# Kernel tuning notes

Hardware: AMD Instinct MI355X
Metric: run time of the kernel (lower is better)

Reference implementation:

```python
import jax, jax.numpy as jnp
import numpy as np

B, N, D = 4, 4096, 256

def setup_inputs() -> dict:
    key = jax.random.key(0)
    ks = jax.random.split(key, 7)
    def xavier(k, shape):
        fan_in, fan_out = shape[1], shape[0]
        a = jnp.sqrt(6.0 / (fan_in + fan_out))
        return jax.random.uniform(k, shape, jnp.float32, -a, a)
    return {
        "x": jax.random.normal(ks[0], (B, N, D), jnp.float32),
        "Wq": xavier(ks[1], (D, D)),
        "bq": jnp.zeros((D,), jnp.float32),
        "Wk": xavier(ks[2], (D, D)),
        "bk": jnp.zeros((D,), jnp.float32),
        "Wv": xavier(ks[3], (D, D)),
        "bv": jnp.zeros((D,), jnp.float32),
        "scale": jnp.asarray([jnp.sqrt(jnp.float32(D))]),
    }

def reference(x, Wq, bq, Wk, bk, Wv, bv, scale):
    # nn.Linear: y = x @ W.T + b
    q = jnp.einsum('bnd,ed->bne', x, Wq) + bq
    k = jnp.einsum('bnd,ed->bne', x, Wk) + bk
    v = jnp.einsum('bnd,ed->bne', x, Wv) + bv
    scores = jnp.einsum('bqd,bkd->bqk', q, k) / scale[0]  # [B,N,N]
    attn = jax.nn.softmax(scores, axis=-1)
    out = jnp.einsum('bqk,bkd->bqd', attn, v)
    return out
```

## Files before the change

### kernel.cpp

```cpp
#include <hip/hip_runtime.h>
#include <hip/hip_bf16.h>

typedef unsigned int u32;
typedef unsigned short u16;
typedef __attribute__((ext_vector_type(8))) __bf16 bf8v;
typedef __attribute__((ext_vector_type(16))) float f32x16;
typedef __attribute__((ext_vector_type(8))) u16 u16x8;

__device__ inline u16 f2bf(float f) {
    u32 u = __float_as_uint(f);
    u = (u + 0x7FFF + ((u >> 16) & 1)) >> 16;
    return (u16)u;
}
__device__ inline u32 pk2(float a, float b) {
    return (u32)f2bf(a) | ((u32)f2bf(b) << 16);
}
__device__ inline float bf2f(u16 h) { return __uint_as_float(((u32)h) << 16); }

__device__ inline u32 cvtpk(float a, float b) {
    u32 r;
    asm("v_cvt_pk_bf16_f32 %0, %1, %2" : "=v"(r) : "v"(a), "v"(b));
    return r;
}
__device__ inline void plswap(u32& a, u32& b) {
    asm("v_permlane32_swap_b32 %0, %1" : "+v"(a), "+v"(b));
}

__device__ inline void dma16(const u16* g, u16* l) {
    __builtin_amdgcn_global_load_lds(
        (const __attribute__((address_space(1))) void*)g,
        (__attribute__((address_space(3))) void*)l, 16, 0, 0);
}

__global__ void cvt_all(const float* __restrict__ x,
                        const float* __restrict__ wq, const float* __restrict__ wk,
                        const float* __restrict__ wv,
                        u16* __restrict__ xp, u16* __restrict__ wall) {
    const int blk = blockIdx.x;
    if (blk < 2048) {
        int g = blk * 256 + threadIdx.x;
        int row = g >> 5, cp = g & 31;
        const float* s = x + row * 256 + cp * 8;
        float4 a = *(const float4*)s;
        float4 b = *(const float4*)(s + 4);
        uint4 o;
        o.x = pk2(a.x, a.y); o.y = pk2(a.z, a.w);
        o.z = pk2(b.x, b.y); o.w = pk2(b.z, b.w);
        *(uint4*)(xp + (row >> 5) * 8192 + cp * 256 + (row & 31) * 8) = o;
    } else {
        const int bb = blk - 2048;
        const int m = bb >> 5;
        const float* src = m == 0 ? wq : m == 1 ? wk : wv;
        int g = (bb & 31) * 256 + threadIdx.x;
        int row = g >> 5, c = g & 31;
        const float* s = src + row * 256 + c * 8;
        float4 a = *(const float4*)s;
        float4 b = *(const float4*)(s + 4);
        uint4 o;
        o.x = pk2(a.x, a.y); o.y = pk2(a.z, a.w);
        o.z = pk2(b.x, b.y); o.w = pk2(b.z, b.w);
        *(uint4*)(wall + m * 65536 + row * 256 + ((c ^ (row & 7)) * 8)) = o;
    }
}

__global__ __launch_bounds__(256) void qkv_proj(
    const u16* __restrict__ xp, const u16* __restrict__ wall,
    const float* __restrict__ bq, const float* __restrict__ bk, const float* __restrict__ bv,
    const float* __restrict__ scale,
    u16* __restrict__ qp, u16* __restrict__ kp, u16* __restrict__ vp)
{
    __shared__ u16 Ws[128 * 256];

    const int blk = blockIdx.x;
    const int xcd = blk & 7;
    const int r2 = blk >> 3;
    const int rt = r2 / 6;
    const int cz = r2 % 6;
    const int sel = cz >> 1;
    const int colbase = (cz & 1) * 128;
    const int rowbase0 = (xcd * 16 + rt) * 128;

    const float* bias = sel == 0 ? bq : sel == 1 ? bk : bv;
    const float qs = sel == 0 ? 1.44269504088896f / scale[0] : 1.0f;
    const int tid = threadIdx.x;
    const int wave = tid >> 6, lane = tid & 63;
    const int l31 = lane & 31, l5 = lane >> 5;
    const int tg = (rowbase0 >> 5) + wave;

    {
        const u16* wsrc = wall + sel * 65536 + colbase * 256;
#pragma unroll
        for (int j = 0; j < 16; j++) {
            const int i = wave * 16 + j;
            dma16(wsrc + i * 512 + lane * 8, Ws + i * 512);
        }
    }
    asm volatile("s_waitcnt vmcnt(0)" ::: "memory");
    __syncthreads();

    f32x16 acc[4];
#pragma unroll
    for (int cb = 0; cb < 4; cb++)
#pragma unroll
        for (int j = 0; j < 16; j++) acc[cb][j] = 0.f;

    const u16* ap = xp + tg * 8192 + l5 * 256 + l31 * 8;
    const int sw = l31 & 7;
#pragma unroll
    for (int kk = 0; kk < 16; kk++) {
        bf8v af = *(const bf8v*)(ap + kk * 512);
        const int co = ((kk * 2 + l5) ^ sw) * 8;
#pragma unroll
        for (int cb = 0; cb < 4; cb++) {
            bf8v bfr = *(const bf8v*)(Ws + (cb * 32 + l31) * 256 + co);
            acc[cb] = __builtin_amdgcn_mfma_f32_32x32x16_bf16(af, bfr, acc[cb], 0, 0, 0);
        }
    }

    if (sel < 2) {
        u16* base = (sel == 0 ? qp : kp) + tg * 8192;
#pragma unroll
        for (int cb = 0; cb < 4; cb++) {
            const int colb = colbase + cb * 32;
            const float bc = bias[colb + l31];
            const int c0 = (colb >> 3) + (l31 >> 3), j0 = l31 & 7;
#pragma unroll
            for (int r = 0; r < 16; r++) {
                const int R = (r & 3) + 8 * (r >> 2) + 4 * l5;
                base[c0 * 256 + R * 8 + j0] = f2bf((acc[cb][r] + bc) * qs);
            }
        }
    } else {
        u16* base = vp + tg * 8192;
#pragma unroll
        for (int cb = 0; cb < 4; cb++) {
            const int colb = colbase + cb * 32;
            const float bc = bias[colb + l31];
            const int d0 = colb + l31;
#pragma unroll
            for (int r = 0; r < 16; r++) {
                const int R = (r & 3) + 8 * (r >> 2) + 4 * l5;
                base[(R >> 3) * 2048 + d0 * 8 + (R & 7)] = f2bf(acc[cb][r] + bc);
            }
        }
    }
}

__global__ __launch_bounds__(256, 2) void flash_attn(
    const u16* __restrict__ qp_, const u16* __restrict__ kp_, const u16* __restrict__ vp_,
    u16* __restrict__ Opb, float* __restrict__ ml)
{
    __shared__ u16 Ks[2 * 8192];
    __shared__ u16 Vs[2 * 8192];

    const int tid = threadIdx.x;
    const int wave = tid >> 6, lane = tid & 63;
    const int l31 = lane & 31, l5 = lane >> 5;

    const int blk = blockIdx.x;
    const int slot = blk >> 3;
    const int g = (blk & 7) * 2 + (slot >> 5);
    const int qtile = slot & 31;
    const int b = g >> 2, s = g & 3;
    const int qbase = qtile * 128 + wave * 32;

    union { u16x8 u; bf8v v; } oneu;
#pragma unroll
    for (int j = 0; j < 8; j++) oneu.u[j] = 0x3F80;
    const bf8v ones = oneu.v;

    bf8v qf[16];
    {
        const u16* qp = qp_ + (b * 128 + qtile * 4 + wave) * 8192 + l31 * 8;
#pragma unroll
        for (int kk = 0; kk < 16; kk++)
            qf[kk] = *(const bf8v*)(qp + (kk * 2 + l5) * 256);
    }

    f32x16 o[8];
#pragma unroll
    for (int i = 0; i < 8; i++)
#pragma unroll
        for (int j = 0; j < 16; j++) o[i][j] = 0.f;
    f32x16 ls;
#pragma unroll
    for (int j = 0; j < 16; j++) ls[j] = 0.f;

    const u16* kbase = kp_ + (b * 128 + s * 32) * 8192;
    const u16* vbase = vp_ + (b * 128 + s * 32) * 8192;

#pragma unroll
    for (int j = 0; j < 4; j++) {
        const int i = wave * 4 + j;
        dma16(kbase + i * 512 + lane * 8, Ks + i * 512);
    }
#pragma unroll
    for (int j = 0; j < 4; j++) {
        const int i = wave * 4 + j;
        dma16(vbase + i * 512 + lane * 8, Vs + i * 512);
    }
#pragma unroll
    for (int j = 0; j < 4; j++) {
        const int i = wave * 4 + j;
        dma16(kbase + 8192 + i * 512 + lane * 8, Ks + 8192 + i * 512);
    }
    asm volatile("s_waitcnt vmcnt(8)" ::: "memory");
    asm volatile("s_barrier" ::: "memory");

    bf8v pf0, pf1;
    {
        f32x16 c0, c1;
#pragma unroll
        for (int j = 0; j < 16; j++) { c0[j] = 0.f; c1[j] = 0.f; }
#pragma unroll
        for (int j = 0; j < 8; j++) {
            bf8v kf0 = *(const bf8v*)(Ks + (j * 2 + l5) * 256 + l31 * 8);
            c0 = __builtin_amdgcn_mfma_f32_32x32x16_bf16(kf0, qf[j], c0, 0, 0, 0);
            bf8v kf1 = *(const bf8v*)(Ks + ((8 + j) * 2 + l5) * 256 + l31 * 8);
            c1 = __builtin_amdgcn_mfma_f32_32x32x16_bf16(kf1, qf[8 + j], c1, 0, 0, 0);
        }
        float e[16];
#pragma unroll
        for (int r = 0; r < 16; r++)
            e[r] = __builtin_amdgcn_exp2f(c0[r] + c1[r]);
        u32 pA = cvtpk(e[0], e[1]), pB = cvtpk(e[2], e[3]);
        u32 pC = cvtpk(e[4], e[5]), pD = cvtpk(e[6], e[7]);
        plswap(pA, pC); plswap(pB, pD);
        u32 pE = cvtpk(e[8], e[9]),  pF = cvtpk(e[10], e[11]);
        u32 pG = cvtpk(e[12], e[13]), pH = cvtpk(e[14], e[15]);
        plswap(pE, pG); plswap(pF, pH);
        union { uint4 u; bf8v v; } u0, u1;
        u0.u = (uint4){pA, pB, pC, pD};
        u1.u = (uint4){pE, pF, pG, pH};
        pf0 = u0.v; pf1 = u1.v;
    }

#pragma unroll 1
    for (int it = 0; it < 31; it++) {
        const int buf = it & 1;
        asm volatile("s_waitcnt vmcnt(0)" ::: "memory");
        asm volatile("s_barrier" ::: "memory");
        {
            const u16* vt_ = vbase + (it + 1) * 8192;
#pragma unroll
            for (int j = 0; j < 4; j++) {
                const int i = wave * 4 + j;
                dma16(vt_ + i * 512 + lane * 8, Vs + (buf ^ 1) * 8192 + i * 512);
            }
            if (it < 30) {
                const u16* kt_ = kbase + (it + 2) * 8192;
#pragma unroll
                for (int j = 0; j < 4; j++) {
                    const int i = wave * 4 + j;
                    dma16(kt_ + i * 512 + lane * 8, Ks + buf * 8192 + i * 512);
                }
            }
        }
        const u16* Kb_ = Ks + (buf ^ 1) * 8192;
        f32x16 c0, c1;
#pragma unroll
        for (int j = 0; j < 16; j++) { c0[j] = 0.f; c1[j] = 0.f; }
#pragma unroll
        for (int j = 0; j < 8; j++) {
            bf8v kf0 = *(const bf8v*)(Kb_ + (j * 2 + l5) * 256 + l31 * 8);
            c0 = __builtin_amdgcn_mfma_f32_32x32x16_bf16(kf0, qf[j], c0, 0, 0, 0);
            bf8v kf1 = *(const bf8v*)(Kb_ + ((8 + j) * 2 + l5) * 256 + l31 * 8);
            c1 = __builtin_amdgcn_mfma_f32_32x32x16_bf16(kf1, qf[8 + j], c1, 0, 0, 0);
        }
        const u16* Vb_ = Vs + buf * 8192;
        ls = __builtin_amdgcn_mfma_f32_32x32x16_bf16(pf0, ones, ls, 0, 0, 0);
        ls = __builtin_amdgcn_mfma_f32_32x32x16_bf16(pf1, ones, ls, 0, 0, 0);
        float e[16];
#pragma unroll
        for (int j = 0; j < 8; j++) {
            bf8v vf0 = *(const bf8v*)(Vb_ + (l5 * 256 + j * 32 + l31) * 8);
            o[j] = __builtin_amdgcn_mfma_f32_32x32x16_bf16(pf0, vf0, o[j], 0, 0, 0);
            e[2 * j] = __builtin_amdgcn_exp2f(c0[2 * j] + c1[2 * j]);
            bf8v vf1 = *(const bf8v*)(Vb_ + ((2 + l5) * 256 + j * 32 + l31) * 8);
            o[j] = __builtin_amdgcn_mfma_f32_32x32x16_bf16(pf1, vf1, o[j], 0, 0, 0);
            e[2 * j + 1] = __builtin_amdgcn_exp2f(c0[2 * j + 1] + c1[2 * j + 1]);
        }
        {
            u32 pA = cvtpk(e[0], e[1]), pB = cvtpk(e[2], e[3]);
            u32 pC = cvtpk(e[4], e[5]), pD = cvtpk(e[6], e[7]);
            plswap(pA, pC); plswap(pB, pD);
            u32 pE = cvtpk(e[8], e[9]),  pF = cvtpk(e[10], e[11]);
            u32 pG = cvtpk(e[12], e[13]), pH = cvtpk(e[14], e[15]);
            plswap(pE, pG); plswap(pF, pH);
            union { uint4 u; bf8v v; } u0, u1;
            u0.u = (uint4){pA, pB, pC, pD};
            u1.u = (uint4){pE, pF, pG, pH};
            pf0 = u0.v; pf1 = u1.v;
        }
    }

    asm volatile("s_waitcnt vmcnt(0)" ::: "memory");
    asm volatile("s_barrier" ::: "memory");
    {
        const u16* Vb_ = Vs + 8192;
        ls = __builtin_amdgcn_mfma_f32_32x32x16_bf16(pf0, ones, ls, 0, 0, 0);
        ls = __builtin_amdgcn_mfma_f32_32x32x16_bf16(pf1, ones, ls, 0, 0, 0);
#pragma unroll
        for (int j = 0; j < 8; j++) {
            bf8v vf0 = *(const bf8v*)(Vb_ + (l5 * 256 + j * 32 + l31) * 8);
            o[j] = __builtin_amdgcn_mfma_f32_32x32x16_bf16(pf0, vf0, o[j], 0, 0, 0);
            bf8v vf1 = *(const bf8v*)(Vb_ + ((2 + l5) * 256 + j * 32 + l31) * 8);
            o[j] = __builtin_amdgcn_mfma_f32_32x32x16_bf16(pf1, vf1, o[j], 0, 0, 0);
        }
    }

    const int rowg = s * 16384 + b * 4096 + qbase;
    u16* ob = Opb + (size_t)rowg * 256;
#pragma unroll
    for (int nb = 0; nb < 8; nb++)
#pragma unroll
        for (int r = 0; r < 16; r++) {
            const int R = (r & 3) + 8 * (r >> 2) + 4 * l5;
            ob[R * 256 + nb * 32 + l31] = f2bf(o[nb][r]);
        }
    if (l31 == 0)
#pragma unroll
        for (int r = 0; r < 16; r++) {
            const int R = (r & 3) + 8 * (r >> 2) + 4 * l5;
            ml[rowg + R] = ls[r];
        }
}

__global__ __launch_bounds__(256) void combine(
    const u16* __restrict__ Opb, const float* __restrict__ ml, float* __restrict__ out)
{
    const int row = blockIdx.x * 4 + (threadIdx.x >> 6);
    const int lane = threadIdx.x & 63;
    const float denom = ml[row] + ml[16384 + row] + ml[32768 + row] + ml[49152 + row];
    float4 acc = {0.f, 0.f, 0.f, 0.f};
#pragma unroll
    for (int si = 0; si < 4; si++) {
        ushort4 v = *(const ushort4*)(Opb + ((size_t)si * 16384 + row) * 256 + lane * 4);
        acc.x += bf2f(v.x); acc.y += bf2f(v.y);
        acc.z += bf2f(v.z); acc.w += bf2f(v.w);
    }
    const float inv = 1.0f / denom;
    acc.x *= inv; acc.y *= inv; acc.z *= inv; acc.w *= inv;
    *((float4*)(out + (size_t)row * 256) + lane) = acc;
}

extern "C" void kernel_launch(void* const* d_in, const int* in_sizes, int n_in,
                              void* d_out, int out_size, void* d_ws, size_t ws_size,
                              hipStream_t stream) {
    const float* x     = (const float*)d_in[0];
    const float* Wq    = (const float*)d_in[1];
    const float* bq    = (const float*)d_in[2];
    const float* Wk    = (const float*)d_in[3];
    const float* bk    = (const float*)d_in[4];
    const float* Wv    = (const float*)d_in[5];
    const float* bv    = (const float*)d_in[6];
    const float* scale = (const float*)d_in[7];
    float* out = (float*)d_out;

    char* ws = (char*)d_ws;
    u16* xp   = (u16*)ws;
    u16* qp   = (u16*)(ws + (8u  << 20));
    u16* kp   = (u16*)(ws + (16u << 20));
    u16* vp   = (u16*)(ws + (24u << 20));
    u16* wall = (u16*)(ws + (32u << 20));
    u16* Opb  = (u16*)(ws + (34u << 20));
    float* ml = (float*)(ws + (66u << 20));

    cvt_all<<<2144, 256, 0, stream>>>(x, Wq, Wk, Wv, xp, wall);
    qkv_proj<<<768, 256, 0, stream>>>(xp, wall, bq, bk, bv, scale, qp, kp, vp);
    flash_attn<<<512, 256, 0, stream>>>(qp, kp, vp, Opb, ml);
    combine<<<4096, 256, 0, stream>>>(Opb, ml, out);
}
```

Before: 178.0 us.

## Fuse all four stages into one persistent kernel with grid barriers

Merges the conversion, QKV projection, flash attention and combine kernels into a single persistent kernel of 512 blocks. Stages are separated by atomic-counter grid barriers, and the counters are reset with a memset before each launch. The aim is to remove the launch overhead and the idle gaps between the four launches. In exchange, the early stages now run as grid-stride loops with fewer blocks, every block waits at each barrier for the slowest one, and the scheme depends on all 512 blocks being resident at once.

```diff
diff --git a/kernel.cpp b/kernel.cpp
--- a/kernel.cpp
+++ b/kernel.cpp
@@ -7,6 +7,8 @@
 typedef __attribute__((ext_vector_type(16))) float f32x16;
 typedef __attribute__((ext_vector_type(8))) u16 u16x8;
 
+#define NBLK 512
+
 __device__ inline u16 f2bf(float f) {
     u32 u = __float_as_uint(f);
     u = (u + 0x7FFF + ((u >> 16) & 1)) >> 16;
@@ -32,255 +34,209 @@
         (__attribute__((address_space(3))) void*)l, 16, 0, 0);
 }
 
-__global__ void cvt_all(const float* __restrict__ x,
-                        const float* __restrict__ wq, const float* __restrict__ wk,
-                        const float* __restrict__ wv,
-                        u16* __restrict__ xp, u16* __restrict__ wall) {
+__device__ inline void gbar(u32* bar, int ph) {
+    __syncthreads();
+    if (threadIdx.x == 0) {
+        __threadfence();
+        atomicAdd(&bar[ph], 1u);
+        while (atomicAdd(&bar[ph], 0u) < NBLK) __builtin_amdgcn_s_sleep(20);
+    }
+    __syncthreads();
+    __threadfence();
+}
+
+__global__ __launch_bounds__(256, 2) void fused(
+    const float* __restrict__ x,
+    const float* __restrict__ wq, const float* __restrict__ bq_,
+    const float* __restrict__ wk, const float* __restrict__ bk_,
+    const float* __restrict__ wv, const float* __restrict__ bv_,
+    const float* __restrict__ scale,
+    u16* __restrict__ xp, u16* __restrict__ wall,
+    u16* __restrict__ qp_, u16* __restrict__ kp_, u16* __restrict__ vp_,
+    u16* __restrict__ Opb, float* __restrict__ ml,
+    float* __restrict__ out, u32* __restrict__ bar)
+{
+    __shared__ u16 smem[32768];
+
     const int blk = blockIdx.x;
-    if (blk < 2048) {
-        int g = blk * 256 + threadIdx.x;
-        int row = g >> 5, cp = g & 31;
-        const float* s = x + row * 256 + cp * 8;
-        float4 a = *(const float4*)s;
-        float4 b = *(const float4*)(s + 4);
-        uint4 o;
-        o.x = pk2(a.x, a.y); o.y = pk2(a.z, a.w);
-        o.z = pk2(b.x, b.y); o.w = pk2(b.z, b.w);
-        *(uint4*)(xp + (row >> 5) * 8192 + cp * 256 + (row & 31) * 8) = o;
-    } else {
-        const int bb = blk - 2048;
-        const int m = bb >> 5;
-        const float* src = m == 0 ? wq : m == 1 ? wk : wv;
-        int g = (bb & 31) * 256 + threadIdx.x;
-        int row = g >> 5, c = g & 31;
-        const float* s = src + row * 256 + c * 8;
-        float4 a = *(const float4*)s;
-        float4 b = *(const float4*)(s + 4);
-        uint4 o;
-        o.x = pk2(a.x, a.y); o.y = pk2(a.z, a.w);
-        o.z = pk2(b.x, b.y); o.w = pk2(b.z, b.w);
-        *(uint4*)(wall + m * 65536 + row * 256 + ((c ^ (row & 7)) * 8)) = o;
-    }
-}
-
-__global__ __launch_bounds__(256) void qkv_proj(
-    const u16* __restrict__ xp, const u16* __restrict__ wall,
-    const float* __restrict__ bq, const float* __restrict__ bk, const float* __restrict__ bv,
-    const float* __restrict__ scale,
-    u16* __restrict__ qp, u16* __restrict__ kp, u16* __restrict__ vp)
-{
-    __shared__ u16 Ws[128 * 256];
-
-    const int blk = blockIdx.x;
-    const int xcd = blk & 7;
-    const int r2 = blk >> 3;
-    const int rt = r2 / 6;
-    const int cz = r2 % 6;
-    const int sel = cz >> 1;
-    const int colbase = (cz & 1) * 128;
-    const int rowbase0 = (xcd * 16 + rt) * 128;
-
-    const float* bias = sel == 0 ? bq : sel == 1 ? bk : bv;
-    const float qs = sel == 0 ? 1.44269504088896f / scale[0] : 1.0f;
     const int tid = threadIdx.x;
     const int wave = tid >> 6, lane = tid & 63;
     const int l31 = lane & 31, l5 = lane >> 5;
-    const int tg = (rowbase0 >> 5) + wave;
+
+    for (int u = blk; u < 2144; u += NBLK) {
+        if (u < 2048) {
+            int g = u * 256 + tid;
+            int row = g >> 5, cp = g & 31;
+            const float* sp = x + row * 256 + cp * 8;
+            float4 a = *(const float4*)sp;
+            float4 b = *(const float4*)(sp + 4);
+            uint4 o;
+            o.x = pk2(a.x, a.y); o.y = pk2(a.z, a.w);
+            o.z = pk2(b.x, b.y); o.w = pk2(b.z, b.w);
+            *(uint4*)(xp + (row >> 5) * 8192 + cp * 256 + (row & 31) * 8) = o;
+        } else {
+            const int bb = u - 2048;
+            const int m = bb >> 5;
+            const float* src = m == 0 ? wq : m == 1 ? wk : wv;
+            int g = (bb & 31) * 256 + tid;
+            int row = g >> 5, c = g & 31;
+            const float* sp = src + row * 256 + c * 8;
+            float4 a = *(const float4*)sp;
+            float4 b = *(const float4*)(sp + 4);
+            uint4 o;
+            o.x = pk2(a.x, a.y); o.y = pk2(a.z, a.w);
+            o.z = pk2(b.x, b.y); o.w = pk2(b.z, b.w);
+            *(uint4*)(wall + m * 65536 + row * 256 + ((c ^ (row & 7)) * 8)) = o;
+        }
+    }
+
+    gbar(bar, 0);
+
+    for (int u = blk; u < 768; u += NBLK) {
+        __syncthreads();
+        const int xcd = u & 7;
+        const int r2 = u >> 3;
+        const int rt = r2 / 6;
+        const int cz = r2 % 6;
+        const int sel = cz >> 1;
+        const int colbase = (cz & 1) * 128;
+        const int rowbase0 = (xcd * 16 + rt) * 128;
+
+        const float* bias = sel == 0 ? bq_ : sel == 1 ? bk_ : bv_;
+        const float qs = sel == 0 ? 1.44269504088896f / scale[0] : 1.0f;
+        const int tg = (rowbase0 >> 5) + wave;
+
+        u16* Ws = smem;
+        {
+            const u16* wsrc = wall + sel * 65536 + colbase * 256;
+#pragma unroll
+            for (int j = 0; j < 16; j++) {
+                const int i = wave * 16 + j;
+                dma16(wsrc + i * 512 + lane * 8, Ws + i * 512);
+            }
+        }
+        asm volatile("s_waitcnt vmcnt(0)" ::: "memory");
+        __syncthreads();
+
+        f32x16 acc[4];
+#pragma unroll
+        for (int cb = 0; cb < 4; cb++)
+#pragma unroll
+            for (int j = 0; j < 16; j++) acc[cb][j] = 0.f;
+
+        const u16* ap = xp + tg * 8192 + l5 * 256 + l31 * 8;
+        const int sw = l31 & 7;
+#pragma unroll
+        for (int kk = 0; kk < 16; kk++) {
+            bf8v af = *(const bf8v*)(ap + kk * 512);
+            const int co = ((kk * 2 + l5) ^ sw) * 8;
+#pragma unroll
+            for (int cb = 0; cb < 4; cb++) {
+                bf8v bfr = *(const bf8v*)(Ws + (cb * 32 + l31) * 256 + co);
+                acc[cb] = __builtin_amdgcn_mfma_f32_32x32x16_bf16(af, bfr, acc[cb], 0, 0, 0);
+            }
+        }
+
+        if (sel < 2) {
+            u16* base = (sel == 0 ? qp_ : kp_) + tg * 8192;
+#pragma unroll
+            for (int cb = 0; cb < 4; cb++) {
+                const int colb = colbase + cb * 32;
+                const float bc = bias[colb + l31];
+                const int c0 = (colb >> 3) + (l31 >> 3), j0 = l31 & 7;
+#pragma unroll
+                for (int r = 0; r < 16; r++) {
+                    const int R = (r & 3) + 8 * (r >> 2) + 4 * l5;
+                    base[c0 * 256 + R * 8 + j0] = f2bf((acc[cb][r] + bc) * qs);
+                }
+            }
+        } else {
+            u16* base = vp_ + tg * 8192;
+#pragma unroll
+            for (int cb = 0; cb < 4; cb++) {
+                const int colb = colbase + cb * 32;
+                const float bc = bias[colb + l31];
+                const int d0 = colb + l31;
+#pragma unroll
+                for (int r = 0; r < 16; r++) {
+                    const int R = (r & 3) + 8 * (r >> 2) + 4 * l5;
+                    base[(R >> 3) * 2048 + d0 * 8 + (R & 7)] = f2bf(acc[cb][r] + bc);
+                }
+            }
+        }
+    }
+
+    gbar(bar, 1);
 
     {
-        const u16* wsrc = wall + sel * 65536 + colbase * 256;
-#pragma unroll
-        for (int j = 0; j < 16; j++) {
-            const int i = wave * 16 + j;
-            dma16(wsrc + i * 512 + lane * 8, Ws + i * 512);
-        }
-    }
-    asm volatile("s_waitcnt vmcnt(0)" ::: "memory");
-    __syncthreads();
-
-    f32x16 acc[4];
-#pragma unroll
-    for (int cb = 0; cb < 4; cb++)
-#pragma unroll
-        for (int j = 0; j < 16; j++) acc[cb][j] = 0.f;
-
-    const u16* ap = xp + tg * 8192 + l5 * 256 + l31 * 8;
-    const int sw = l31 & 7;
-#pragma unroll
-    for (int kk = 0; kk < 16; kk++) {
-        bf8v af = *(const bf8v*)(ap + kk * 512);
-        const int co = ((kk * 2 + l5) ^ sw) * 8;
-#pragma unroll
-        for (int cb = 0; cb < 4; cb++) {
-            bf8v bfr = *(const bf8v*)(Ws + (cb * 32 + l31) * 256 + co);
-            acc[cb] = __builtin_amdgcn_mfma_f32_32x32x16_bf16(af, bfr, acc[cb], 0, 0, 0);
-        }
-    }
-
-    if (sel < 2) {
-        u16* base = (sel == 0 ? qp : kp) + tg * 8192;
-#pragma unroll
-        for (int cb = 0; cb < 4; cb++) {
-            const int colb = colbase + cb * 32;
-            const float bc = bias[colb + l31];
-            const int c0 = (colb >> 3) + (l31 >> 3), j0 = l31 & 7;
-#pragma unroll
-            for (int r = 0; r < 16; r++) {
-                const int R = (r & 3) + 8 * (r >> 2) + 4 * l5;
-                base[c0 * 256 + R * 8 + j0] = f2bf((acc[cb][r] + bc) * qs);
-            }
-        }
-    } else {
-        u16* base = vp + tg * 8192;
-#pragma unroll
-        for (int cb = 0; cb < 4; cb++) {
-            const int colb = colbase + cb * 32;
-            const float bc = bias[colb + l31];
-            const int d0 = colb + l31;
-#pragma unroll
-            for (int r = 0; r < 16; r++) {
-                const int R = (r & 3) + 8 * (r >> 2) + 4 * l5;
-                base[(R >> 3) * 2048 + d0 * 8 + (R & 7)] = f2bf(acc[cb][r] + bc);
-            }
-        }
-    }
-}
-
-__global__ __launch_bounds__(256, 2) void flash_attn(
-    const u16* __restrict__ qp_, const u16* __restrict__ kp_, const u16* __restrict__ vp_,
-    u16* __restrict__ Opb, float* __restrict__ ml)
-{
-    __shared__ u16 Ks[2 * 8192];
-    __shared__ u16 Vs[2 * 8192];
-
-    const int tid = threadIdx.x;
-    const int wave = tid >> 6, lane = tid & 63;
-    const int l31 = lane & 31, l5 = lane >> 5;
-
-    const int blk = blockIdx.x;
-    const int slot = blk >> 3;
-    const int g = (blk & 7) * 2 + (slot >> 5);
-    const int qtile = slot & 31;
-    const int b = g >> 2, s = g & 3;
-    const int qbase = qtile * 128 + wave * 32;
-
-    union { u16x8 u; bf8v v; } oneu;
-#pragma unroll
-    for (int j = 0; j < 8; j++) oneu.u[j] = 0x3F80;
-    const bf8v ones = oneu.v;
-
-    bf8v qf[16];
-    {
-        const u16* qp = qp_ + (b * 128 + qtile * 4 + wave) * 8192 + l31 * 8;
-#pragma unroll
-        for (int kk = 0; kk < 16; kk++)
-            qf[kk] = *(const bf8v*)(qp + (kk * 2 + l5) * 256);
-    }
-
-    f32x16 o[8];
-#pragma unroll
-    for (int i = 0; i < 8; i++)
-#pragma unroll
-        for (int j = 0; j < 16; j++) o[i][j] = 0.f;
-    f32x16 ls;
-#pragma unroll
-    for (int j = 0; j < 16; j++) ls[j] = 0.f;
-
-    const u16* kbase = kp_ + (b * 128 + s * 32) * 8192;
-    const u16* vbase = vp_ + (b * 128 + s * 32) * 8192;
-
-#pragma unroll
-    for (int j = 0; j < 4; j++) {
-        const int i = wave * 4 + j;
-        dma16(kbase + i * 512 + lane * 8, Ks + i * 512);
-    }
-#pragma unroll
-    for (int j = 0; j < 4; j++) {
-        const int i = wave * 4 + j;
-        dma16(vbase + i * 512 + lane * 8, Vs + i * 512);
-    }
-#pragma unroll
-    for (int j = 0; j < 4; j++) {
-        const int i = wave * 4 + j;
-        dma16(kbase + 8192 + i * 512 + lane * 8, Ks + 8192 + i * 512);
-    }
-    asm volatile("s_waitcnt vmcnt(8)" ::: "memory");
-    asm volatile("s_barrier" ::: "memory");
-
-    bf8v pf0, pf1;
-    {
-        f32x16 c0, c1;
-#pragma unroll
-        for (int j = 0; j < 16; j++) { c0[j] = 0.f; c1[j] = 0.f; }
-#pragma unroll
-        for (int j = 0; j < 8; j++) {
-            bf8v kf0 = *(const bf8v*)(Ks + (j * 2 + l5) * 256 + l31 * 8);
-            c0 = __builtin_amdgcn_mfma_f32_32x32x16_bf16(kf0, qf[j], c0, 0, 0, 0);
-            bf8v kf1 = *(const bf8v*)(Ks + ((8 + j) * 2 + l5) * 256 + l31 * 8);
-            c1 = __builtin_amdgcn_mfma_f32_32x32x16_bf16(kf1, qf[8 + j], c1, 0, 0, 0);
-        }
-        float e[16];
-#pragma unroll
-        for (int r = 0; r < 16; r++)
-            e[r] = __builtin_amdgcn_exp2f(c0[r] + c1[r]);
-        u32 pA = cvtpk(e[0], e[1]), pB = cvtpk(e[2], e[3]);
-        u32 pC = cvtpk(e[4], e[5]), pD = cvtpk(e[6], e[7]);
-        plswap(pA, pC); plswap(pB, pD);
-        u32 pE = cvtpk(e[8], e[9]),  pF = cvtpk(e[10], e[11]);
-        u32 pG = cvtpk(e[12], e[13]), pH = cvtpk(e[14], e[15]);
-        plswap(pE, pG); plswap(pF, pH);
-        union { uint4 u; bf8v v; } u0, u1;
-        u0.u = (uint4){pA, pB, pC, pD};
-        u1.u = (uint4){pE, pF, pG, pH};
-        pf0 = u0.v; pf1 = u1.v;
-    }
-
-#pragma unroll 1
-    for (int it = 0; it < 31; it++) {
-        const int buf = it & 1;
-        asm volatile("s_waitcnt vmcnt(0)" ::: "memory");
+        u16* Ks = smem;
+        u16* Vs = smem + 16384;
+
+        const int slot = blk >> 3;
+        const int g = (blk & 7) * 2 + (slot >> 5);
+        const int qtile = slot & 31;
+        const int b = g >> 2, s = g & 3;
+        const int qbase = qtile * 128 + wave * 32;
+
+        union { u16x8 u; bf8v v; } oneu;
+#pragma unroll
+        for (int j = 0; j < 8; j++) oneu.u[j] = 0x3F80;
+        const bf8v ones = oneu.v;
+
+        bf8v qf[16];
+        {
+            const u16* qp = qp_ + (b * 128 + qtile * 4 + wave) * 8192 + l31 * 8;
+#pragma unroll
+            for (int kk = 0; kk < 16; kk++)
+                qf[kk] = *(const bf8v*)(qp + (kk * 2 + l5) * 256);
+        }
+
+        f32x16 o[8];
+#pragma unroll
+        for (int i = 0; i < 8; i++)
+#pragma unroll
+            for (int j = 0; j < 16; j++) o[i][j] = 0.f;
+        f32x16 ls;
+#pragma unroll
+        for (int j = 0; j < 16; j++) ls[j] = 0.f;
+
+        const u16* kbase = kp_ + (b * 128 + s * 32) * 8192;
+        const u16* vbase = vp_ + (b * 128 + s * 32) * 8192;
+
+#pragma unroll
+        for (int j = 0; j < 4; j++) {
+            const int i = wave * 4 + j;
+            dma16(kbase + i * 512 + lane * 8, Ks + i * 512);
+        }
+#pragma unroll
+        for (int j = 0; j < 4; j++) {
+            const int i = wave * 4 + j;
+            dma16(vbase + i * 512 + lane * 8, Vs + i * 512);
+        }
+#pragma unroll
+        for (int j = 0; j < 4; j++) {
+            const int i = wave * 4 + j;
+            dma16(kbase + 8192 + i * 512 + lane * 8, Ks + 8192 + i * 512);
+        }
+        asm volatile("s_waitcnt vmcnt(8)" ::: "memory");
         asm volatile("s_barrier" ::: "memory");
+
+        bf8v pf0, pf1;
         {
-            const u16* vt_ = vbase + (it + 1) * 8192;
-#pragma unroll
-            for (int j = 0; j < 4; j++) {
-                const int i = wave * 4 + j;
-                dma16(vt_ + i * 512 + lane * 8, Vs + (buf ^ 1) * 8192 + i * 512);
-            }
-            if (it < 30) {
-                const u16* kt_ = kbase + (it + 2) * 8192;
-#pragma unroll
-                for (int j = 0; j < 4; j++) {
-                    const int i = wave * 4 + j;
-                    dma16(kt_ + i * 512 + lane * 8, Ks + buf * 8192 + i * 512);
-                }
-            }
-        }
-        const u16* Kb_ = Ks + (buf ^ 1) * 8192;
-        f32x16 c0, c1;
-#pragma unroll
-        for (int j = 0; j < 16; j++) { c0[j] = 0.f; c1[j] = 0.f; }
-#pragma unroll
-        for (int j = 0; j < 8; j++) {
-            bf8v kf0 = *(const bf8v*)(Kb_ + (j * 2 + l5) * 256 + l31 * 8);
-            c0 = __builtin_amdgcn_mfma_f32_32x32x16_bf16(kf0, qf[j], c0, 0, 0, 0);
-            bf8v kf1 = *(const bf8v*)(Kb_ + ((8 + j) * 2 + l5) * 256 + l31 * 8);
-            c1 = __builtin_amdgcn_mfma_f32_32x32x16_bf16(kf1, qf[8 + j], c1, 0, 0, 0);
-        }
-        const u16* Vb_ = Vs + buf * 8192;
-        ls = __builtin_amdgcn_mfma_f32_32x32x16_bf16(pf0, ones, ls, 0, 0, 0);
-        ls = __builtin_amdgcn_mfma_f32_32x32x16_bf16(pf1, ones, ls, 0, 0, 0);
-        float e[16];
-#pragma unroll
-        for (int j = 0; j < 8; j++) {
-            bf8v vf0 = *(const bf8v*)(Vb_ + (l5 * 256 + j * 32 + l31) * 8);
-            o[j] = __builtin_amdgcn_mfma_f32_32x32x16_bf16(pf0, vf0, o[j], 0, 0, 0);
-            e[2 * j] = __builtin_amdgcn_exp2f(c0[2 * j] + c1[2 * j]);
-            bf8v vf1 = *(const bf8v*)(Vb_ + ((2 + l5) * 256 + j * 32 + l31) * 8);
-            o[j] = __builtin_amdgcn_mfma_f32_32x32x16_bf16(pf1, vf1, o[j], 0, 0, 0);
-            e[2 * j + 1] = __builtin_amdgcn_exp2f(c0[2 * j + 1] + c1[2 * j + 1]);
-        }
-        {
+            f32x16 c0, c1;
+#pragma unroll
+            for (int j = 0; j < 16; j++) { c0[j] = 0.f; c1[j] = 0.f; }
+#pragma unroll
+            for (int j = 0; j < 8; j++) {
+                bf8v kf0 = *(const bf8v*)(Ks + (j * 2 + l5) * 256 + l31 * 8);
+                c0 = __builtin_amdgcn_mfma_f32_32x32x16_bf16(kf0, qf[j], c0, 0, 0, 0);
+                bf8v kf1 = *(const bf8v*)(Ks + ((8 + j) * 2 + l5) * 256 + l31 * 8);
+                c1 = __builtin_amdgcn_mfma_f32_32x32x16_bf16(kf1, qf[8 + j], c1, 0, 0, 0);
+            }
+            float e[16];
+#pragma unroll
+            for (int r = 0; r < 16; r++)
+                e[r] = __builtin_amdgcn_exp2f(c0[r] + c1[r]);
             u32 pA = cvtpk(e[0], e[1]), pB = cvtpk(e[2], e[3]);
             u32 pC = cvtpk(e[4], e[5]), pD = cvtpk(e[6], e[7]);
             plswap(pA, pC); plswap(pB, pD);
@@ -292,56 +248,115 @@
             u1.u = (uint4){pE, pF, pG, pH};
             pf0 = u0.v; pf1 = u1.v;
         }
-    }
-
-    asm volatile("s_waitcnt vmcnt(0)" ::: "memory");
-    asm volatile("s_barrier" ::: "memory");
-    {
-        const u16* Vb_ = Vs + 8192;
-        ls = __builtin_amdgcn_mfma_f32_32x32x16_bf16(pf0, ones, ls, 0, 0, 0);
-        ls = __builtin_amdgcn_mfma_f32_32x32x16_bf16(pf1, ones, ls, 0, 0, 0);
-#pragma unroll
-        for (int j = 0; j < 8; j++) {
-            bf8v vf0 = *(const bf8v*)(Vb_ + (l5 * 256 + j * 32 + l31) * 8);
-            o[j] = __builtin_amdgcn_mfma_f32_32x32x16_bf16(pf0, vf0, o[j], 0, 0, 0);
-            bf8v vf1 = *(const bf8v*)(Vb_ + ((2 + l5) * 256 + j * 32 + l31) * 8);
-            o[j] = __builtin_amdgcn_mfma_f32_32x32x16_bf16(pf1, vf1, o[j], 0, 0, 0);
-        }
-    }
-
-    const int rowg = s * 16384 + b * 4096 + qbase;
-    u16* ob = Opb + (size_t)rowg * 256;
-#pragma unroll
-    for (int nb = 0; nb < 8; nb++)
-#pragma unroll
-        for (int r = 0; r < 16; r++) {
-            const int R = (r & 3) + 8 * (r >> 2) + 4 * l5;
-            ob[R * 256 + nb * 32 + l31] = f2bf(o[nb][r]);
-        }
-    if (l31 == 0)
-#pragma unroll
-        for (int r = 0; r < 16; r++) {
-            const int R = (r & 3) + 8 * (r >> 2) + 4 * l5;
-            ml[rowg + R] = ls[r];
-        }
-}
-
-__global__ __launch_bounds__(256) void combine(
-    const u16* __restrict__ Opb, const float* __restrict__ ml, float* __restrict__ out)
-{
-    const int row = blockIdx.x * 4 + (threadIdx.x >> 6);
-    const int lane = threadIdx.x & 63;
-    const float denom = ml[row] + ml[16384 + row] + ml[32768 + row] + ml[49152 + row];
-    float4 acc = {0.f, 0.f, 0.f, 0.f};
-#pragma unroll
-    for (int si = 0; si < 4; si++) {
-        ushort4 v = *(const ushort4*)(Opb + ((size_t)si * 16384 + row) * 256 + lane * 4);
-        acc.x += bf2f(v.x); acc.y += bf2f(v.y);
-        acc.z += bf2f(v.z); acc.w += bf2f(v.w);
-    }
-    const float inv = 1.0f / denom;
-    acc.x *= inv; acc.y *= inv; acc.z *= inv; acc.w *= inv;
-    *((float4*)(out + (size_t)row * 256) + lane) = acc;
+
+#pragma unroll 1
+        for (int it = 0; it < 31; it++) {
+            const int buf = it & 1;
+            asm volatile("s_waitcnt vmcnt(0)" ::: "memory");
+            asm volatile("s_barrier" ::: "memory");
+            {
+                const u16* vt_ = vbase + (it + 1) * 8192;
+#pragma unroll
+                for (int j = 0; j < 4; j++) {
+                    const int i = wave * 4 + j;
+                    dma16(vt_ + i * 512 + lane * 8, Vs + (buf ^ 1) * 8192 + i * 512);
+                }
+                if (it < 30) {
+                    const u16* kt_ = kbase + (it + 2) * 8192;
+#pragma unroll
+                    for (int j = 0; j < 4; j++) {
+                        const int i = wave * 4 + j;
+                        dma16(kt_ + i * 512 + lane * 8, Ks + buf * 8192 + i * 512);
+                    }
+                }
+            }
+            const u16* Kb_ = Ks + (buf ^ 1) * 8192;
+            f32x16 c0, c1;
+#pragma unroll
+            for (int j = 0; j < 16; j++) { c0[j] = 0.f; c1[j] = 0.f; }
+#pragma unroll
+            for (int j = 0; j < 8; j++) {
+                bf8v kf0 = *(const bf8v*)(Kb_ + (j * 2 + l5) * 256 + l31 * 8);
+                c0 = __builtin_amdgcn_mfma_f32_32x32x16_bf16(kf0, qf[j], c0, 0, 0, 0);
+                bf8v kf1 = *(const bf8v*)(Kb_ + ((8 + j) * 2 + l5) * 256 + l31 * 8);
+                c1 = __builtin_amdgcn_mfma_f32_32x32x16_bf16(kf1, qf[8 + j], c1, 0, 0, 0);
+            }
+            const u16* Vb_ = Vs + buf * 8192;
+            ls = __builtin_amdgcn_mfma_f32_32x32x16_bf16(pf0, ones, ls, 0, 0, 0);
+            ls = __builtin_amdgcn_mfma_f32_32x32x16_bf16(pf1, ones, ls, 0, 0, 0);
+            float e[16];
+#pragma unroll
+            for (int j = 0; j < 8; j++) {
+                bf8v vf0 = *(const bf8v*)(Vb_ + (l5 * 256 + j * 32 + l31) * 8);
+                o[j] = __builtin_amdgcn_mfma_f32_32x32x16_bf16(pf0, vf0, o[j], 0, 0, 0);
+                e[2 * j] = __builtin_amdgcn_exp2f(c0[2 * j] + c1[2 * j]);
+                bf8v vf1 = *(const bf8v*)(Vb_ + ((2 + l5) * 256 + j * 32 + l31) * 8);
+                o[j] = __builtin_amdgcn_mfma_f32_32x32x16_bf16(pf1, vf1, o[j], 0, 0, 0);
+                e[2 * j + 1] = __builtin_amdgcn_exp2f(c0[2 * j + 1] + c1[2 * j + 1]);
+            }
+            {
+                u32 pA = cvtpk(e[0], e[1]), pB = cvtpk(e[2], e[3]);
+                u32 pC = cvtpk(e[4], e[5]), pD = cvtpk(e[6], e[7]);
+                plswap(pA, pC); plswap(pB, pD);
+                u32 pE = cvtpk(e[8], e[9]),  pF = cvtpk(e[10], e[11]);
+                u32 pG = cvtpk(e[12], e[13]), pH = cvtpk(e[14], e[15]);
+                plswap(pE, pG); plswap(pF, pH);
+                union { uint4 u; bf8v v; } u0, u1;
+                u0.u = (uint4){pA, pB, pC, pD};
+                u1.u = (uint4){pE, pF, pG, pH};
+                pf0 = u0.v; pf1 = u1.v;
+            }
+        }
+
+        asm volatile("s_waitcnt vmcnt(0)" ::: "memory");
+        asm volatile("s_barrier" ::: "memory");
+        {
+            const u16* Vb_ = Vs + 8192;
+            ls = __builtin_amdgcn_mfma_f32_32x32x16_bf16(pf0, ones, ls, 0, 0, 0);
+            ls = __builtin_amdgcn_mfma_f32_32x32x16_bf16(pf1, ones, ls, 0, 0, 0);
+#pragma unroll
+            for (int j = 0; j < 8; j++) {
+                bf8v vf0 = *(const bf8v*)(Vb_ + (l5 * 256 + j * 32 + l31) * 8);
+                o[j] = __builtin_amdgcn_mfma_f32_32x32x16_bf16(pf0, vf0, o[j], 0, 0, 0);
+                bf8v vf1 = *(const bf8v*)(Vb_ + ((2 + l5) * 256 + j * 32 + l31) * 8);
+                o[j] = __builtin_amdgcn_mfma_f32_32x32x16_bf16(pf1, vf1, o[j], 0, 0, 0);
+            }
+        }
+
+        const int rowg = s * 16384 + b * 4096 + qbase;
+        u16* ob = Opb + (size_t)rowg * 256;
+#pragma unroll
+        for (int nb = 0; nb < 8; nb++)
+#pragma unroll
+            for (int r = 0; r < 16; r++) {
+                const int R = (r & 3) + 8 * (r >> 2) + 4 * l5;
+                ob[R * 256 + nb * 32 + l31] = f2bf(o[nb][r]);
+            }
+        if (l31 == 0)
+#pragma unroll
+            for (int r = 0; r < 16; r++) {
+                const int R = (r & 3) + 8 * (r >> 2) + 4 * l5;
+                ml[rowg + R] = ls[r];
+            }
+    }
+
+    gbar(bar, 2);
+
+#pragma unroll 1
+    for (int rr = 0; rr < 8; rr++) {
+        const int row = blk * 32 + rr * 4 + wave;
+        const float denom = ml[row] + ml[16384 + row] + ml[32768 + row] + ml[49152 + row];
+        float4 acc = {0.f, 0.f, 0.f, 0.f};
+#pragma unroll
+        for (int si = 0; si < 4; si++) {
+            ushort4 v = *(const ushort4*)(Opb + ((size_t)si * 16384 + row) * 256 + lane * 4);
+            acc.x += bf2f(v.x); acc.y += bf2f(v.y);
+            acc.z += bf2f(v.z); acc.w += bf2f(v.w);
+        }
+        const float inv = 1.0f / denom;
+        acc.x *= inv; acc.y *= inv; acc.z *= inv; acc.w *= inv;
+        *((float4*)(out + (size_t)row * 256) + lane) = acc;
+    }
 }
 
 extern "C" void kernel_launch(void* const* d_in, const int* in_sizes, int n_in,
@@ -365,9 +380,9 @@
     u16* wall = (u16*)(ws + (32u << 20));
     u16* Opb  = (u16*)(ws + (34u << 20));
     float* ml = (float*)(ws + (66u << 20));
-
-    cvt_all<<<2144, 256, 0, stream>>>(x, Wq, Wk, Wv, xp, wall);
-    qkv_proj<<<768, 256, 0, stream>>>(xp, wall, bq, bk, bv, scale, qp, kp, vp);
-    flash_attn<<<512, 256, 0, stream>>>(qp, kp, vp, Opb, ml);
-    combine<<<4096, 256, 0, stream>>>(Opb, ml, out);
-}
+    u32* bar  = (u32*)(ws + (67u << 20));
+
+    hipMemsetAsync(bar, 0, 64, stream);
+    fused<<<NBLK, 256, 0, stream>>>(x, Wq, bq, Wk, bk, Wv, bv, scale,
+                                    xp, wall, qp, kp, vp, Opb, ml, out, bar);
+}
```

New measurement: 408.7 us. 2.3x slower.

## Replace MFMA row-sum with VALU exp accumulation and vectorize projection stores

Applied to the files above, without the earlier changes.

The softmax denominator was computed by extra MFMA ops that multiplied P by a ones matrix. It is now accumulated as a per-lane fp32 sum of the exponentials and combined across the two lane halves with a permlane swap at the end. This removes two MFMAs per iteration and sums in fp32 instead of bf16-rounded P, at the cost of a few VALU adds. The Q/K projection swaps its MFMA operand order so each lane holds contiguous columns, which lets the projection epilogues write packed 4-element bf16 stores instead of scalar 16-bit stores.

```diff
diff --git a/kernel.cpp b/kernel.cpp
--- a/kernel.cpp
+++ b/kernel.cpp
@@ -106,31 +106,43 @@
 
     const u16* ap = xp + tg * 8192 + l5 * 256 + l31 * 8;
     const int sw = l31 & 7;
-#pragma unroll
-    for (int kk = 0; kk < 16; kk++) {
-        bf8v af = *(const bf8v*)(ap + kk * 512);
-        const int co = ((kk * 2 + l5) ^ sw) * 8;
-#pragma unroll
-        for (int cb = 0; cb < 4; cb++) {
-            bf8v bfr = *(const bf8v*)(Ws + (cb * 32 + l31) * 256 + co);
-            acc[cb] = __builtin_amdgcn_mfma_f32_32x32x16_bf16(af, bfr, acc[cb], 0, 0, 0);
-        }
-    }
-
     if (sel < 2) {
+#pragma unroll
+        for (int kk = 0; kk < 16; kk++) {
+            bf8v af = *(const bf8v*)(ap + kk * 512);
+            const int co = ((kk * 2 + l5) ^ sw) * 8;
+#pragma unroll
+            for (int cb = 0; cb < 4; cb++) {
+                bf8v bfr = *(const bf8v*)(Ws + (cb * 32 + l31) * 256 + co);
+                acc[cb] = __builtin_amdgcn_mfma_f32_32x32x16_bf16(bfr, af, acc[cb], 0, 0, 0);
+            }
+        }
         u16* base = (sel == 0 ? qp : kp) + tg * 8192;
 #pragma unroll
         for (int cb = 0; cb < 4; cb++) {
             const int colb = colbase + cb * 32;
-            const float bc = bias[colb + l31];
-            const int c0 = (colb >> 3) + (l31 >> 3), j0 = l31 & 7;
-#pragma unroll
-            for (int r = 0; r < 16; r++) {
-                const int R = (r & 3) + 8 * (r >> 2) + 4 * l5;
-                base[c0 * 256 + R * 8 + j0] = f2bf((acc[cb][r] + bc) * qs);
+#pragma unroll
+            for (int q = 0; q < 4; q++) {
+                const float4 b4 = *(const float4*)(bias + colb + 8 * q + 4 * l5);
+                const float v0 = (acc[cb][4 * q + 0] + b4.x) * qs;
+                const float v1 = (acc[cb][4 * q + 1] + b4.y) * qs;
+                const float v2 = (acc[cb][4 * q + 2] + b4.z) * qs;
+                const float v3 = (acc[cb][4 * q + 3] + b4.w) * qs;
+                uint2 o2 = { cvtpk(v0, v1), cvtpk(v2, v3) };
+                *(uint2*)(base + ((colb >> 3) + q) * 256 + l31 * 8 + 4 * l5) = o2;
             }
         }
     } else {
+#pragma unroll
+        for (int kk = 0; kk < 16; kk++) {
+            bf8v af = *(const bf8v*)(ap + kk * 512);
+            const int co = ((kk * 2 + l5) ^ sw) * 8;
+#pragma unroll
+            for (int cb = 0; cb < 4; cb++) {
+                bf8v bfr = *(const bf8v*)(Ws + (cb * 32 + l31) * 256 + co);
+                acc[cb] = __builtin_amdgcn_mfma_f32_32x32x16_bf16(af, bfr, acc[cb], 0, 0, 0);
+            }
+        }
         u16* base = vp + tg * 8192;
 #pragma unroll
         for (int cb = 0; cb < 4; cb++) {
@@ -138,9 +150,13 @@
             const float bc = bias[colb + l31];
             const int d0 = colb + l31;
 #pragma unroll
-            for (int r = 0; r < 16; r++) {
-                const int R = (r & 3) + 8 * (r >> 2) + 4 * l5;
-                base[(R >> 3) * 2048 + d0 * 8 + (R & 7)] = f2bf(acc[cb][r] + bc);
+            for (int q = 0; q < 4; q++) {
+                const float v0 = acc[cb][4 * q + 0] + bc;
+                const float v1 = acc[cb][4 * q + 1] + bc;
+                const float v2 = acc[cb][4 * q + 2] + bc;
+                const float v3 = acc[cb][4 * q + 3] + bc;
+                uint2 o2 = { cvtpk(v0, v1), cvtpk(v2, v3) };
+                *(uint2*)(base + q * 2048 + d0 * 8 + 4 * l5) = o2;
             }
         }
     }
@@ -164,11 +180,6 @@
     const int b = g >> 2, s = g & 3;
     const int qbase = qtile * 128 + wave * 32;
 
-    union { u16x8 u; bf8v v; } oneu;
-#pragma unroll
-    for (int j = 0; j < 8; j++) oneu.u[j] = 0x3F80;
-    const bf8v ones = oneu.v;
-
     bf8v qf[16];
     {
         const u16* qp = qp_ + (b * 128 + qtile * 4 + wave) * 8192 + l31 * 8;
@@ -182,9 +193,7 @@
     for (int i = 0; i < 8; i++)
 #pragma unroll
         for (int j = 0; j < 16; j++) o[i][j] = 0.f;
-    f32x16 ls;
-#pragma unroll
-    for (int j = 0; j < 16; j++) ls[j] = 0.f;
+    float lsum = 0.f;
 
     const u16* kbase = kp_ + (b * 128 + s * 32) * 8192;
     const u16* vbase = vp_ + (b * 128 + s * 32) * 8192;
@@ -223,6 +232,13 @@
 #pragma unroll
         for (int r = 0; r < 16; r++)
             e[r] = __builtin_amdgcn_exp2f(c0[r] + c1[r]);
+        {
+            float s0 = (e[0] + e[1]) + (e[2] + e[3]);
+            float s1 = (e[4] + e[5]) + (e[6] + e[7]);
+            float s2 = (e[8] + e[9]) + (e[10] + e[11]);
+            float s3 = (e[12] + e[13]) + (e[14] + e[15]);
+            lsum += (s0 + s1) + (s2 + s3);
+        }
         u32 pA = cvtpk(e[0], e[1]), pB = cvtpk(e[2], e[3]);
         u32 pC = cvtpk(e[4], e[5]), pD = cvtpk(e[6], e[7]);
         plswap(pA, pC); plswap(pB, pD);
@@ -268,8 +284,6 @@
             c1 = __builtin_amdgcn_mfma_f32_32x32x16_bf16(kf1, qf[8 + j], c1, 0, 0, 0);
         }
         const u16* Vb_ = Vs + buf * 8192;
-        ls = __builtin_amdgcn_mfma_f32_32x32x16_bf16(pf0, ones, ls, 0, 0, 0);
-        ls = __builtin_amdgcn_mfma_f32_32x32x16_bf16(pf1, ones, ls, 0, 0, 0);
         float e[16];
 #pragma unroll
         for (int j = 0; j < 8; j++) {
@@ -279,6 +293,13 @@
             bf8v vf1 = *(const bf8v*)(Vb_ + ((2 + l5) * 256 + j * 32 + l31) * 8);
             o[j] = __builtin_amdgcn_mfma_f32_32x32x16_bf16(pf1, vf1, o[j], 0, 0, 0);
             e[2 * j + 1] = __builtin_amdgcn_exp2f(c0[2 * j + 1] + c1[2 * j + 1]);
+        }
+        {
+            float s0 = (e[0] + e[1]) + (e[2] + e[3]);
+            float s1 = (e[4] + e[5]) + (e[6] + e[7]);
+            float s2 = (e[8] + e[9]) + (e[10] + e[11]);
+            float s3 = (e[12] + e[13]) + (e[14] + e[15]);
+            lsum += (s0 + s1) + (s2 + s3);
         }
         {
             u32 pA = cvtpk(e[0], e[1]), pB = cvtpk(e[2], e[3]);
@@ -298,8 +319,6 @@
     asm volatile("s_barrier" ::: "memory");
     {
         const u16* Vb_ = Vs + 8192;
-        ls = __builtin_amdgcn_mfma_f32_32x32x16_bf16(pf0, ones, ls, 0, 0, 0);
-        ls = __builtin_amdgcn_mfma_f32_32x32x16_bf16(pf1, ones, ls, 0, 0, 0);
 #pragma unroll
         for (int j = 0; j < 8; j++) {
             bf8v vf0 = *(const bf8v*)(Vb_ + (l5 * 256 + j * 32 + l31) * 8);
@@ -318,12 +337,12 @@
             const int R = (r & 3) + 8 * (r >> 2) + 4 * l5;
             ob[R * 256 + nb * 32 + l31] = f2bf(o[nb][r]);
         }
-    if (l31 == 0)
-#pragma unroll
-        for (int r = 0; r < 16; r++) {
-            const int R = (r & 3) + 8 * (r >> 2) + 4 * l5;
-            ml[rowg + R] = ls[r];
-        }
+    {
+        u32 a = __float_as_uint(lsum), b2 = a;
+        plswap(a, b2);
+        const float tot = lsum + __uint_as_float(l5 ? a : b2);
+        if (l5 == 0) ml[rowg + l31] = tot;
+    }
 }
 
 __global__ __launch_bounds__(256) void combine(
```

Result: faster. 170.6 us (-4.1%).
